# Kernel tuning notes

Hardware: AMD Instinct MI355X
Metric: run time of the kernel (lower is better)

The kernel has to match this reference:

```python
import jax, jax.numpy as jnp
import numpy as np

N_NODES = 1_000_000
N_EDGES = 16_000_000
F_IN, F_H1, F_H2, N_CLS = 32, 16, 8, 5
N_GRAPHS = 10_000


def setup_inputs() -> dict:
    key = jax.random.key(0)
    ks = jax.random.split(key, 10)
    x = jax.random.normal(ks[0], (N_NODES, F_IN), dtype=jnp.float32)
    edge_index = jax.random.randint(ks[1], (2, N_EDGES), 0, N_NODES, dtype=jnp.int32)
    batch = jnp.sort(jax.random.randint(ks[2], (N_NODES,), 0, N_GRAPHS, dtype=jnp.int32))
    # learned params (Glorot-ish scale)
    W1 = jax.random.normal(ks[3], (F_IN, F_H1), dtype=jnp.float32) / np.sqrt(F_IN)
    b1 = jnp.zeros((F_H1,), dtype=jnp.float32)
    W2 = jax.random.normal(ks[4], (F_H1, F_H2), dtype=jnp.float32) / np.sqrt(F_H1)
    b2 = jnp.zeros((F_H2,), dtype=jnp.float32)
    Wl = jax.random.normal(ks[5], (F_H2, N_CLS), dtype=jnp.float32) / np.sqrt(F_H2)
    bl = jnp.zeros((N_CLS,), dtype=jnp.float32)
    return {"x": x, "edge_index": edge_index, "batch": batch, "num_graphs": N_GRAPHS,
            "W1": W1, "b1": b1, "W2": W2, "b2": b2, "Wl": Wl, "bl": bl}


def _gcn_conv(x, W, b, src, dst, deg_inv_sqrt, norm_e, num_nodes):
    # h = X W, then symmetric-normalized aggregation with self loops:
    # out_i = sum_{(j->i)} norm_ji * h_j + deg_i^{-1} * h_i + b
    h = x @ W                                  # [N, F_out]
    msg = h[src] * norm_e[:, None]             # [E, F_out] gather + scale
    agg = jax.ops.segment_sum(msg, dst, num_segments=num_nodes)
    self_loop = h * (deg_inv_sqrt * deg_inv_sqrt)[:, None]
    return agg + self_loop + b


def reference(x, edge_index, batch, num_graphs, W1, b1, W2, b2, Wl, bl):
    num_nodes = x.shape[0]
    src, dst = edge_index[0], edge_index[1]
    # degrees including self loops (GCN: A_hat = A + I)
    deg = jax.ops.segment_sum(jnp.ones_like(dst, dtype=x.dtype), dst,
                              num_segments=num_nodes) + 1.0
    deg_inv_sqrt = jax.lax.rsqrt(deg)
    norm_e = deg_inv_sqrt[src] * deg_inv_sqrt[dst]   # [E]

    h = _gcn_conv(x, W1, b1, src, dst, deg_inv_sqrt, norm_e, num_nodes)
    h = jax.nn.relu(h)
    h = _gcn_conv(h, W2, b2, src, dst, deg_inv_sqrt, norm_e, num_nodes)
    h = jax.nn.relu(h)

    # global_mean_pool over graph ids
    sums = jax.ops.segment_sum(h, batch, num_segments=num_graphs)     # [G, F_H2]
    cnts = jax.ops.segment_sum(jnp.ones((num_nodes,), dtype=h.dtype), batch,
                               num_segments=num_graphs)
    pooled = sums / jnp.maximum(cnts, 1.0)[:, None]
    return pooled @ Wl + bl
```

## Files before the change

kernel.cpp:

```cpp
#include <hip/hip_runtime.h>


namespace {

constexpr int F_IN = 32, F_H1 = 16, F_H2 = 8, N_CLS = 5;
constexpr int BB = 10, NPB = 1 << BB;
constexpr int MAXB = 1024;
constexpr int CHUNK = 12288;


__global__ void k_mm1(const float* __restrict__ x, const float* __restrict__ W,
                      float* __restrict__ h, int N) {
  __shared__ float w[F_IN * F_H1];
  for (int k = threadIdx.x; k < F_IN * F_H1; k += blockDim.x) w[k] = W[k];
  __syncthreads();
  int i = blockIdx.x * blockDim.x + threadIdx.x;
  if (i >= N) return;
  const float4* xr = reinterpret_cast<const float4*>(x + (size_t)i * F_IN);
  float acc[F_H1];
#pragma unroll
  for (int f = 0; f < F_H1; ++f) acc[f] = 0.f;
#pragma unroll
  for (int k4 = 0; k4 < F_IN / 4; ++k4) {
    float4 v = xr[k4];
    float vv[4] = {v.x, v.y, v.z, v.w};
#pragma unroll
    for (int j = 0; j < 4; ++j) {
      const float* wr = &w[(k4 * 4 + j) * F_H1];
#pragma unroll
      for (int f = 0; f < F_H1; ++f) acc[f] = fmaf(vv[j], wr[f], acc[f]);
    }
  }
  float4* hr = reinterpret_cast<float4*>(h + (size_t)i * F_H1);
#pragma unroll
  for (int q = 0; q < F_H1 / 4; ++q)
    hr[q] = make_float4(acc[q * 4], acc[q * 4 + 1], acc[q * 4 + 2], acc[q * 4 + 3]);
}

__global__ void k_mm2(const float* __restrict__ in, const float* __restrict__ W,
                      float* __restrict__ h, int N) {
  __shared__ float w[F_H1 * F_H2];
  for (int k = threadIdx.x; k < F_H1 * F_H2; k += blockDim.x) w[k] = W[k];
  __syncthreads();
  int i = blockIdx.x * blockDim.x + threadIdx.x;
  if (i >= N) return;
  const float4* xr = reinterpret_cast<const float4*>(in + (size_t)i * F_H1);
  float acc[F_H2];
#pragma unroll
  for (int f = 0; f < F_H2; ++f) acc[f] = 0.f;
#pragma unroll
  for (int k4 = 0; k4 < F_H1 / 4; ++k4) {
    float4 v = xr[k4];
    float vv[4] = {v.x, v.y, v.z, v.w};
#pragma unroll
    for (int j = 0; j < 4; ++j) {
      const float* wr = &w[(k4 * 4 + j) * F_H2];
#pragma unroll
      for (int f = 0; f < F_H2; ++f) acc[f] = fmaf(vv[j], wr[f], acc[f]);
    }
  }
  float4* hr = reinterpret_cast<float4*>(h + (size_t)i * F_H2);
#pragma unroll
  for (int q = 0; q < F_H2 / 4; ++q)
    hr[q] = make_float4(acc[q * 4], acc[q * 4 + 1], acc[q * 4 + 2], acc[q * 4 + 3]);
}

__global__ void k_final(const float* __restrict__ pooled, const float* __restrict__ cnts,
                        const float* __restrict__ Wl, const float* __restrict__ bl,
                        float* __restrict__ out, int total) {
  int gid = blockIdx.x * blockDim.x + threadIdx.x;
  if (gid >= total) return;
  int g = gid / N_CLS, c = gid % N_CLS;
  float s = 0.f;
#pragma unroll
  for (int f = 0; f < F_H2; ++f) s += pooled[g * F_H2 + f] * Wl[f * N_CLS + c];
  out[gid] = s / fmaxf(cnts[g], 1.f) + bl[c];
}


__global__ void k_hist(const int* __restrict__ dst, int* __restrict__ bcnt,
                       int E, int nbuck) {
  __shared__ int h[MAXB];
  for (int i = threadIdx.x; i < MAXB; i += blockDim.x) h[i] = 0;
  __syncthreads();
  for (int e = blockIdx.x * blockDim.x + threadIdx.x; e < E;
       e += gridDim.x * blockDim.x)
    atomicAdd(&h[dst[e] >> BB], 1);
  __syncthreads();
  for (int i = threadIdx.x; i < nbuck; i += blockDim.x)
    if (h[i]) atomicAdd(&bcnt[i], h[i]);
}

__global__ void k_bscan(const int* __restrict__ bcnt, int* __restrict__ bbase,
                        int* __restrict__ bcur, int nbuck, int E) {
  __shared__ int s[MAXB];
  int t = threadIdx.x;
  int v = (t < nbuck) ? bcnt[t] : 0;
  s[t] = v;
  __syncthreads();
  for (int off = 1; off < MAXB; off <<= 1) {
    int x = (t >= off) ? s[t - off] : 0;
    __syncthreads();
    s[t] += x;
    __syncthreads();
  }
  int ex = s[t] - v;
  if (t < nbuck) { bbase[t] = ex; bcur[t] = ex; }
  if (t == 0) bbase[nbuck] = E;
}

__global__ __launch_bounds__(256)
void k_binscatter(const int* __restrict__ dst, const int* __restrict__ src,
                  int* __restrict__ bcur, int* __restrict__ packed, int E) {
  __shared__ int hist[MAXB];
  __shared__ int sbase[MAXB];
  __shared__ int lcur[MAXB];
  __shared__ int stg[CHUNK];
  __shared__ int stmp[256];
  int t = threadIdx.x;
  int c0 = blockIdx.x * CHUNK;
  int n = min(CHUNK, E - c0);
  for (int i = t; i < MAXB; i += 256) hist[i] = 0;
  __syncthreads();
  for (int j = t; j < n; j += 256) atomicAdd(&hist[dst[c0 + j] >> BB], 1);
  __syncthreads();
  int v[4], sum = 0;
  int b4 = t * 4;
#pragma unroll
  for (int k = 0; k < 4; ++k) { v[k] = hist[b4 + k]; sum += v[k]; }
  stmp[t] = sum;
  __syncthreads();
  for (int off = 1; off < 256; off <<= 1) {
    int x = (t >= off) ? stmp[t - off] : 0;
    __syncthreads();
    stmp[t] += x;
    __syncthreads();
  }
  int run = stmp[t] - sum;
#pragma unroll
  for (int k = 0; k < 4; ++k) { sbase[b4 + k] = run; lcur[b4 + k] = run; run += v[k]; }
  __syncthreads();
  for (int i = t; i < MAXB; i += 256) {
    int c = hist[i];
    if (c) hist[i] = atomicAdd(&bcur[i], c);
  }
  __syncthreads();
  for (int j = t; j < n; j += 256) {
    int d = dst[c0 + j], s = src[c0 + j];
    int b = d >> BB;
    int p = atomicAdd(&lcur[b], 1);
    stg[p] = ((d & (NPB - 1)) << 20) | s;
  }
  __syncthreads();
  for (int j = t; j < n; j += 256) {
    int lo = 0, hi = MAXB - 1;
    while (lo < hi) {
      int mid = (lo + hi + 1) >> 1;
      if (sbase[mid] <= j) lo = mid; else hi = mid - 1;
    }
    packed[hist[lo] + (j - sbase[lo])] = stg[j];
  }
}

__global__ void k_dis_b(const int* __restrict__ bbase, const int* __restrict__ packed,
                        float* __restrict__ dis, int N) {
  __shared__ int cnt[NPB];
  int t = threadIdx.x;
  for (int i = t; i < NPB; i += blockDim.x) cnt[i] = 0;
  __syncthreads();
  int b = blockIdx.x;
  int beg = bbase[b], end = bbase[b + 1];
  for (int e = beg + t; e < end; e += blockDim.x)
    atomicAdd(&cnt[packed[e] >> 20], 1);
  __syncthreads();
  int node0 = b << BB;
  for (int i = t; i < NPB; i += blockDim.x) {
    int node = node0 + i;
    if (node < N) dis[node] = rsqrtf((float)cnt[i] + 1.0f);
  }
}


template <int F>
__global__ __launch_bounds__(512)
void k_conv(const int* __restrict__ bbase, const int* __restrict__ packed,
            const float* __restrict__ dis, const float* __restrict__ h,
            const float* __restrict__ bias, float* __restrict__ out, int N) {
  __shared__ float acc[NPB * F];
  int t = threadIdx.x;
  for (int i = t; i < NPB * F; i += 512) acc[i] = 0.f;
  __syncthreads();
  int b = blockIdx.x;
  int beg = bbase[b], end = bbase[b + 1];
  const int EPI = 512 / F;
  int f = t % F, eg = t / F;
  for (int e = beg + eg; e < end; e += 2 * EPI) {
    int p0 = packed[e];
    int s0 = p0 & ((1 << 20) - 1), d0 = p0 >> 20;
    float m0 = dis[s0] * h[(size_t)s0 * F + f];
    int e1 = e + EPI;
    if (e1 < end) {
      int p1 = packed[e1];
      int s1 = p1 & ((1 << 20) - 1), d1 = p1 >> 20;
      float m1 = dis[s1] * h[(size_t)s1 * F + f];
      atomicAdd(&acc[d0 * F + f], m0);
      atomicAdd(&acc[d1 * F + f], m1);
    } else {
      atomicAdd(&acc[d0 * F + f], m0);
    }
  }
  __syncthreads();
  int node0 = b << BB;
  for (int i = t; i < NPB * F; i += 512) {
    int node = node0 + i / F;
    if (node >= N) continue;
    int ff = i % F;
    float di = dis[node];
    float v = fmaf(di, acc[i], fmaf(di * di, h[(size_t)node * F + ff], bias[ff]));
    out[(size_t)node * F + ff] = fmaxf(v, 0.f);
  }
}

__global__ __launch_bounds__(512)
void k_conv_pool(const int* __restrict__ bbase, const int* __restrict__ packed,
                 const float* __restrict__ dis, const float* __restrict__ h,
                 const float* __restrict__ bias, const int* __restrict__ batch,
                 float* __restrict__ pooled, float* __restrict__ cnts, int N) {
  constexpr int F = F_H2;
  __shared__ float acc[NPB * F];
  int t = threadIdx.x;
  for (int i = t; i < NPB * F; i += 512) acc[i] = 0.f;
  __syncthreads();
  int b = blockIdx.x;
  int beg = bbase[b], end = bbase[b + 1];
  const int EPI = 512 / F;
  int f = t % F, eg = t / F;
  for (int e = beg + eg; e < end; e += 2 * EPI) {
    int p0 = packed[e];
    int s0 = p0 & ((1 << 20) - 1), d0 = p0 >> 20;
    float m0 = dis[s0] * h[(size_t)s0 * F + f];
    int e1 = e + EPI;
    if (e1 < end) {
      int p1 = packed[e1];
      int s1 = p1 & ((1 << 20) - 1), d1 = p1 >> 20;
      float m1 = dis[s1] * h[(size_t)s1 * F + f];
      atomicAdd(&acc[d0 * F + f], m0);
      atomicAdd(&acc[d1 * F + f], m1);
    } else {
      atomicAdd(&acc[d0 * F + f], m0);
    }
  }
  __syncthreads();
  int node0 = b << BB;
  for (int i = t; i < NPB * F; i += 512) {
    int node = node0 + i / F;
    if (node >= N) continue;
    int ff = i % F;
    float di = dis[node];
    float v = fmaf(di, acc[i], fmaf(di * di, h[(size_t)node * F + ff], bias[ff]));
    v = fmaxf(v, 0.f);
    int g = batch[node];
    atomicAdd(&pooled[g * F_H2 + ff], v);
    if (ff == 0) atomicAdd(&cnts[g], 1.0f);
  }
}


__global__ void k_deg(const int* __restrict__ dst, float* __restrict__ deg, int E) {
  int e = blockIdx.x * blockDim.x + threadIdx.x;
  if (e < E) atomicAdd(&deg[dst[e]], 1.0f);
}
__global__ void k_dis(float* __restrict__ d, int N) {
  int i = blockIdx.x * blockDim.x + threadIdx.x;
  if (i < N) d[i] = rsqrtf(d[i] + 1.0f);
}
template <int F>
__global__ void k_edge(const int* __restrict__ src, const int* __restrict__ dst,
                       const float* __restrict__ dis, const float* __restrict__ h,
                       float* __restrict__ agg, int total) {
  int gid = blockIdx.x * blockDim.x + threadIdx.x;
  if (gid >= total) return;
  int e = gid / F, f = gid % F;
  int s = src[e], d = dst[e];
  atomicAdd(&agg[d * F + f], h[s * F + f] * dis[s] * dis[d]);
}
template <int F>
__global__ void k_combine(const float* __restrict__ h, const float* __restrict__ dis,
                          const float* __restrict__ b, float* __restrict__ agg, int total) {
  int gid = blockIdx.x * blockDim.x + threadIdx.x;
  if (gid >= total) return;
  int i = gid / F, f = gid % F;
  float di = dis[i];
  agg[gid] = fmaxf(agg[gid] + h[gid] * di * di + b[f], 0.f);
}
__global__ void k_combine_pool_fb(const float* __restrict__ h2, const float* __restrict__ agg2,
                                  const float* __restrict__ dis, const float* __restrict__ b,
                                  const int* __restrict__ batch, float* __restrict__ pooled,
                                  float* __restrict__ cnts, int total) {
  int gid = blockIdx.x * blockDim.x + threadIdx.x;
  if (gid >= total) return;
  int i = gid >> 3, f = gid & 7;
  float di = dis[i];
  float v = fmaxf(agg2[gid] + h2[gid] * di * di + b[f], 0.f);
  int g = batch[i];
  atomicAdd(&pooled[g * F_H2 + f], v);
  if (f == 0) atomicAdd(&cnts[g], 1.0f);
}

}

extern "C" void kernel_launch(void* const* d_in, const int* in_sizes, int n_in,
                              void* d_out, int out_size, void* d_ws, size_t ws_size,
                              hipStream_t stream) {
  const float* x   = (const float*)d_in[0];
  const int* ei    = (const int*)d_in[1];
  const int* batch = (const int*)d_in[2];
  const float* W1 = (const float*)d_in[4];
  const float* b1 = (const float*)d_in[5];
  const float* W2 = (const float*)d_in[6];
  const float* b2 = (const float*)d_in[7];
  const float* Wl = (const float*)d_in[8];
  const float* bl = (const float*)d_in[9];

  const int N = in_sizes[0] / F_IN;
  const int E = in_sizes[1] / 2;
  const int G = out_size / N_CLS;
  const int* src  = ei;
  const int* dstp = ei + E;

  const int BLK = 256;
  const int nbuck = (N + NPB - 1) >> BB;

  size_t need = (size_t)(3 * MAXB + 8) * 4
              + (size_t)E * 4
              + (size_t)N * 4
              + (size_t)N * F_H1 * 4
              + (size_t)N * F_H1 * 4
              + (size_t)G * (F_H2 + 1) * 4 + 1024;

  if (N <= (1 << 20) && nbuck <= MAXB && ws_size >= need) {
    char* p = (char*)d_ws;
    int*   bcnt   = (int*)p;    p += (size_t)MAXB * 4;
    int*   bbase  = (int*)p;    p += (size_t)(MAXB + 4) * 4;
    int*   bcur   = (int*)p;    p += (size_t)MAXB * 4;
    int*   packed = (int*)p;    p += (size_t)E * 4;
    float* dis    = (float*)p;  p += (size_t)N * 4;
    float* H      = (float*)p;  p += (size_t)N * F_H1 * 4;
    float* O      = (float*)p;  p += (size_t)N * F_H1 * 4;
    float* pooled = (float*)p;  p += (size_t)G * F_H2 * 4;
    float* cnts   = (float*)p;

    hipMemsetAsync(bcnt, 0, (size_t)MAXB * 4, stream);
    hipMemsetAsync(pooled, 0, ((size_t)G * F_H2 + G) * 4, stream);

    k_hist<<<2048, BLK, 0, stream>>>(dstp, bcnt, E, nbuck);
    k_bscan<<<1, MAXB, 0, stream>>>(bcnt, bbase, bcur, nbuck, E);
    k_binscatter<<<(E + CHUNK - 1) / CHUNK, BLK, 0, stream>>>(dstp, src, bcur, packed, E);
    k_dis_b<<<nbuck, BLK, 0, stream>>>(bbase, packed, dis, N);

    k_mm1<<<(N + BLK - 1) / BLK, BLK, 0, stream>>>(x, W1, H, N);
    k_conv<F_H1><<<nbuck, 512, 0, stream>>>(bbase, packed, dis, H, b1, O, N);
    k_mm2<<<(N + BLK - 1) / BLK, BLK, 0, stream>>>(O, W2, H, N);
    k_conv_pool<<<nbuck, 512, 0, stream>>>(bbase, packed, dis, H, b2, batch,
                                           pooled, cnts, N);

    k_final<<<(G * N_CLS + BLK - 1) / BLK, BLK, 0, stream>>>(
        pooled, cnts, Wl, bl, (float*)d_out, G * N_CLS);
    return;
  }

  float* ws = (float*)d_ws;
  float* dis    = ws;
  float* A      = ws + N;
  float* B      = A + (size_t)N * F_H1;
  float* h2     = A;
  float* agg2   = A + (size_t)N * F_H2;
  float* pooled = B + (size_t)N * F_H1;
  float* cnts   = pooled + (size_t)G * F_H2;

  hipMemsetAsync(dis, 0, (size_t)N * sizeof(float), stream);
  hipMemsetAsync(B, 0, (size_t)N * F_H1 * sizeof(float), stream);
  hipMemsetAsync(pooled, 0, ((size_t)G * F_H2 + G) * sizeof(float), stream);

  k_deg<<<(E + BLK - 1) / BLK, BLK, 0, stream>>>(dstp, dis, E);
  k_dis<<<(N + BLK - 1) / BLK, BLK, 0, stream>>>(dis, N);
  k_mm1<<<(N + BLK - 1) / BLK, BLK, 0, stream>>>(x, W1, A, N);
  k_edge<F_H1><<<(E * F_H1 + BLK - 1) / BLK, BLK, 0, stream>>>(src, dstp, dis, A, B, E * F_H1);
  k_combine<F_H1><<<(N * F_H1 + BLK - 1) / BLK, BLK, 0, stream>>>(A, dis, b1, B, N * F_H1);
  hipMemsetAsync(agg2, 0, (size_t)N * F_H2 * sizeof(float), stream);
  k_mm2<<<(N + BLK - 1) / BLK, BLK, 0, stream>>>(B, W2, h2, N);
  k_edge<F_H2><<<(E * F_H2 + BLK - 1) / BLK, BLK, 0, stream>>>(src, dstp, dis, h2, agg2, E * F_H2);
  k_combine_pool_fb<<<(N * F_H2 + BLK - 1) / BLK, BLK, 0, stream>>>(
      h2, agg2, dis, b2, batch, pooled, cnts, N * F_H2);
  k_final<<<(G * N_CLS + BLK - 1) / BLK, BLK, 0, stream>>>(
      pooled, cnts, Wl, bl, (float*)d_out, G * N_CLS);
}
```

Baseline: 2.882 ms.

## Prescale features by inverse-sqrt degree, shrink buckets, unroll gathers, add nontemporal loads

The matmul kernels now multiply each node's output row by its inverse-sqrt degree, so the edge loop gathers only the prescaled feature and no longer reads dis per source. The shared accumulator starts from the node's own prescaled row, which makes the self-loop term fall out of the algebra. Bucket width drops to 512 nodes with 2048 buckets and smaller scatter chunks, the scan is adapted to cover them, and the edge loop is unrolled four-deep to keep more gathers in flight. Nontemporal loads and stores and an occupancy launch bound are added, which may change cache behaviour and register pressure.

```diff
diff --git a/kernel.cpp b/kernel.cpp
--- a/kernel.cpp
+++ b/kernel.cpp
@@ -4,25 +4,27 @@
 namespace {
 
 constexpr int F_IN = 32, F_H1 = 16, F_H2 = 8, N_CLS = 5;
-constexpr int BB = 10, NPB = 1 << BB;
-constexpr int MAXB = 1024;
-constexpr int CHUNK = 12288;
+constexpr int BB = 9, NPB = 1 << BB;
+constexpr int MAXB = 2048;
+constexpr int CHUNK = 8192;
+
+typedef float v4f __attribute__((ext_vector_type(4)));
 
 
 __global__ void k_mm1(const float* __restrict__ x, const float* __restrict__ W,
-                      float* __restrict__ h, int N) {
+                      const float* __restrict__ dis, float* __restrict__ hp, int N) {
   __shared__ float w[F_IN * F_H1];
   for (int k = threadIdx.x; k < F_IN * F_H1; k += blockDim.x) w[k] = W[k];
   __syncthreads();
   int i = blockIdx.x * blockDim.x + threadIdx.x;
   if (i >= N) return;
-  const float4* xr = reinterpret_cast<const float4*>(x + (size_t)i * F_IN);
+  const v4f* xr = reinterpret_cast<const v4f*>(x + (size_t)i * F_IN);
   float acc[F_H1];
 #pragma unroll
   for (int f = 0; f < F_H1; ++f) acc[f] = 0.f;
 #pragma unroll
   for (int k4 = 0; k4 < F_IN / 4; ++k4) {
-    float4 v = xr[k4];
+    v4f v = __builtin_nontemporal_load(&xr[k4]);
     float vv[4] = {v.x, v.y, v.z, v.w};
 #pragma unroll
     for (int j = 0; j < 4; ++j) {
@@ -31,26 +33,33 @@
       for (int f = 0; f < F_H1; ++f) acc[f] = fmaf(vv[j], wr[f], acc[f]);
     }
   }
-  float4* hr = reinterpret_cast<float4*>(h + (size_t)i * F_H1);
-#pragma unroll
-  for (int q = 0; q < F_H1 / 4; ++q)
-    hr[q] = make_float4(acc[q * 4], acc[q * 4 + 1], acc[q * 4 + 2], acc[q * 4 + 3]);
+  float di = dis ? dis[i] : 1.f;
+  v4f* hr = reinterpret_cast<v4f*>(hp + (size_t)i * F_H1);
+#pragma unroll
+  for (int q = 0; q < F_H1 / 4; ++q) {
+    v4f r;
+    r.x = di * acc[q * 4];
+    r.y = di * acc[q * 4 + 1];
+    r.z = di * acc[q * 4 + 2];
+    r.w = di * acc[q * 4 + 3];
+    hr[q] = r;
+  }
 }
 
 __global__ void k_mm2(const float* __restrict__ in, const float* __restrict__ W,
-                      float* __restrict__ h, int N) {
+                      const float* __restrict__ dis, float* __restrict__ hp, int N) {
   __shared__ float w[F_H1 * F_H2];
   for (int k = threadIdx.x; k < F_H1 * F_H2; k += blockDim.x) w[k] = W[k];
   __syncthreads();
   int i = blockIdx.x * blockDim.x + threadIdx.x;
   if (i >= N) return;
-  const float4* xr = reinterpret_cast<const float4*>(in + (size_t)i * F_H1);
+  const v4f* xr = reinterpret_cast<const v4f*>(in + (size_t)i * F_H1);
   float acc[F_H2];
 #pragma unroll
   for (int f = 0; f < F_H2; ++f) acc[f] = 0.f;
 #pragma unroll
   for (int k4 = 0; k4 < F_H1 / 4; ++k4) {
-    float4 v = xr[k4];
+    v4f v = __builtin_nontemporal_load(&xr[k4]);
     float vv[4] = {v.x, v.y, v.z, v.w};
 #pragma unroll
     for (int j = 0; j < 4; ++j) {
@@ -59,10 +68,17 @@
       for (int f = 0; f < F_H2; ++f) acc[f] = fmaf(vv[j], wr[f], acc[f]);
     }
   }
-  float4* hr = reinterpret_cast<float4*>(h + (size_t)i * F_H2);
-#pragma unroll
-  for (int q = 0; q < F_H2 / 4; ++q)
-    hr[q] = make_float4(acc[q * 4], acc[q * 4 + 1], acc[q * 4 + 2], acc[q * 4 + 3]);
+  float di = dis ? dis[i] : 1.f;
+  v4f* hr = reinterpret_cast<v4f*>(hp + (size_t)i * F_H2);
+#pragma unroll
+  for (int q = 0; q < F_H2 / 4; ++q) {
+    v4f r;
+    r.x = di * acc[q * 4];
+    r.y = di * acc[q * 4 + 1];
+    r.z = di * acc[q * 4 + 2];
+    r.w = di * acc[q * 4 + 3];
+    hr[q] = r;
+  }
 }
 
 __global__ void k_final(const float* __restrict__ pooled, const float* __restrict__ cnts,
@@ -85,7 +101,7 @@
   __syncthreads();
   for (int e = blockIdx.x * blockDim.x + threadIdx.x; e < E;
        e += gridDim.x * blockDim.x)
-    atomicAdd(&h[dst[e] >> BB], 1);
+    atomicAdd(&h[__builtin_nontemporal_load(&dst[e]) >> BB], 1);
   __syncthreads();
   for (int i = threadIdx.x; i < nbuck; i += blockDim.x)
     if (h[i]) atomicAdd(&bcnt[i], h[i]);
@@ -93,19 +109,23 @@
 
 __global__ void k_bscan(const int* __restrict__ bcnt, int* __restrict__ bbase,
                         int* __restrict__ bcur, int nbuck, int E) {
-  __shared__ int s[MAXB];
+  __shared__ int stmp[1024];
   int t = threadIdx.x;
-  int v = (t < nbuck) ? bcnt[t] : 0;
-  s[t] = v;
-  __syncthreads();
-  for (int off = 1; off < MAXB; off <<= 1) {
-    int x = (t >= off) ? s[t - off] : 0;
+  int i0 = t * 2;
+  int v0 = (i0 < nbuck) ? bcnt[i0] : 0;
+  int v1 = (i0 + 1 < nbuck) ? bcnt[i0 + 1] : 0;
+  int sum = v0 + v1;
+  stmp[t] = sum;
+  __syncthreads();
+  for (int off = 1; off < 1024; off <<= 1) {
+    int x = (t >= off) ? stmp[t - off] : 0;
     __syncthreads();
-    s[t] += x;
+    stmp[t] += x;
     __syncthreads();
   }
-  int ex = s[t] - v;
-  if (t < nbuck) { bbase[t] = ex; bcur[t] = ex; }
+  int run = stmp[t] - sum;
+  if (i0 < nbuck) { bbase[i0] = run; bcur[i0] = run; }
+  if (i0 + 1 < nbuck) { bbase[i0 + 1] = run + v0; bcur[i0 + 1] = run + v0; }
   if (t == 0) bbase[nbuck] = E;
 }
 
@@ -122,12 +142,13 @@
   int n = min(CHUNK, E - c0);
   for (int i = t; i < MAXB; i += 256) hist[i] = 0;
   __syncthreads();
-  for (int j = t; j < n; j += 256) atomicAdd(&hist[dst[c0 + j] >> BB], 1);
-  __syncthreads();
-  int v[4], sum = 0;
-  int b4 = t * 4;
-#pragma unroll
-  for (int k = 0; k < 4; ++k) { v[k] = hist[b4 + k]; sum += v[k]; }
+  for (int j = t; j < n; j += 256)
+    atomicAdd(&hist[__builtin_nontemporal_load(&dst[c0 + j]) >> BB], 1);
+  __syncthreads();
+  int v[8], sum = 0;
+  int b8 = t * 8;
+#pragma unroll
+  for (int k = 0; k < 8; ++k) { v[k] = hist[b8 + k]; sum += v[k]; }
   stmp[t] = sum;
   __syncthreads();
   for (int off = 1; off < 256; off <<= 1) {
@@ -138,7 +159,7 @@
   }
   int run = stmp[t] - sum;
 #pragma unroll
-  for (int k = 0; k < 4; ++k) { sbase[b4 + k] = run; lcur[b4 + k] = run; run += v[k]; }
+  for (int k = 0; k < 8; ++k) { sbase[b8 + k] = run; lcur[b8 + k] = run; run += v[k]; }
   __syncthreads();
   for (int i = t; i < MAXB; i += 256) {
     int c = hist[i];
@@ -146,7 +167,8 @@
   }
   __syncthreads();
   for (int j = t; j < n; j += 256) {
-    int d = dst[c0 + j], s = src[c0 + j];
+    int d = __builtin_nontemporal_load(&dst[c0 + j]);
+    int s = __builtin_nontemporal_load(&src[c0 + j]);
     int b = d >> BB;
     int p = atomicAdd(&lcur[b], 1);
     stg[p] = ((d & (NPB - 1)) << 20) | s;
@@ -171,7 +193,7 @@
   int b = blockIdx.x;
   int beg = bbase[b], end = bbase[b + 1];
   for (int e = beg + t; e < end; e += blockDim.x)
-    atomicAdd(&cnt[packed[e] >> 20], 1);
+    atomicAdd(&cnt[__builtin_nontemporal_load(&packed[e]) >> 20], 1);
   __syncthreads();
   int node0 = b << BB;
   for (int i = t; i < NPB; i += blockDim.x) {
@@ -182,83 +204,106 @@
 
 
 template <int F>
-__global__ __launch_bounds__(512)
+__global__ __launch_bounds__(512, 8)
 void k_conv(const int* __restrict__ bbase, const int* __restrict__ packed,
-            const float* __restrict__ dis, const float* __restrict__ h,
+            const float* __restrict__ dis, const float* __restrict__ hp,
             const float* __restrict__ bias, float* __restrict__ out, int N) {
   __shared__ float acc[NPB * F];
   int t = threadIdx.x;
-  for (int i = t; i < NPB * F; i += 512) acc[i] = 0.f;
-  __syncthreads();
   int b = blockIdx.x;
+  int node0 = b << BB;
+  for (int i4 = t; i4 < NPB * F / 4; i4 += 512) {
+    int idx = i4 * 4;
+    int node = node0 + idx / F;
+    v4f v = {0.f, 0.f, 0.f, 0.f};
+    if (node < N) v = *reinterpret_cast<const v4f*>(hp + (size_t)node0 * F + idx);
+    *reinterpret_cast<v4f*>(&acc[idx]) = v;
+  }
+  __syncthreads();
   int beg = bbase[b], end = bbase[b + 1];
   const int EPI = 512 / F;
   int f = t % F, eg = t / F;
-  for (int e = beg + eg; e < end; e += 2 * EPI) {
-    int p0 = packed[e];
-    int s0 = p0 & ((1 << 20) - 1), d0 = p0 >> 20;
-    float m0 = dis[s0] * h[(size_t)s0 * F + f];
-    int e1 = e + EPI;
-    if (e1 < end) {
-      int p1 = packed[e1];
-      int s1 = p1 & ((1 << 20) - 1), d1 = p1 >> 20;
-      float m1 = dis[s1] * h[(size_t)s1 * F + f];
-      atomicAdd(&acc[d0 * F + f], m0);
-      atomicAdd(&acc[d1 * F + f], m1);
-    } else {
-      atomicAdd(&acc[d0 * F + f], m0);
-    }
-  }
-  __syncthreads();
+  for (int e = beg + eg; e < end; e += 4 * EPI) {
+    int pe[4]; float hv[4]; int dl[4]; bool ok[4];
+#pragma unroll
+    for (int u = 0; u < 4; ++u) {
+      int ee = e + u * EPI;
+      ok[u] = ee < end;
+      pe[u] = ok[u] ? __builtin_nontemporal_load(&packed[ee]) : 0;
+    }
+#pragma unroll
+    for (int u = 0; u < 4; ++u) {
+      int s = pe[u] & 0xFFFFF;
+      dl[u] = pe[u] >> 20;
+      hv[u] = ok[u] ? hp[(size_t)s * F + f] : 0.f;
+    }
+#pragma unroll
+    for (int u = 0; u < 4; ++u)
+      if (ok[u]) atomicAdd(&acc[dl[u] * F + f], hv[u]);
+  }
+  __syncthreads();
+  for (int i4 = t; i4 < NPB * F / 4; i4 += 512) {
+    int idx = i4 * 4;
+    int node = node0 + idx / F;
+    if (node >= N) continue;
+    int ff = idx % F;
+    float di = dis[node];
+    v4f a = *reinterpret_cast<const v4f*>(&acc[idx]);
+    v4f r;
+    r.x = fmaxf(fmaf(di, a.x, bias[ff + 0]), 0.f);
+    r.y = fmaxf(fmaf(di, a.y, bias[ff + 1]), 0.f);
+    r.z = fmaxf(fmaf(di, a.z, bias[ff + 2]), 0.f);
+    r.w = fmaxf(fmaf(di, a.w, bias[ff + 3]), 0.f);
+    __builtin_nontemporal_store(r, reinterpret_cast<v4f*>(out + (size_t)node0 * F + idx));
+  }
+}
+
+__global__ __launch_bounds__(512, 8)
+void k_conv_pool(const int* __restrict__ bbase, const int* __restrict__ packed,
+                 const float* __restrict__ dis, const float* __restrict__ hp,
+                 const float* __restrict__ bias, const int* __restrict__ batch,
+                 float* __restrict__ pooled, float* __restrict__ cnts, int N) {
+  constexpr int F = F_H2;
+  __shared__ float acc[NPB * F];
+  int t = threadIdx.x;
+  int b = blockIdx.x;
   int node0 = b << BB;
+  for (int i4 = t; i4 < NPB * F / 4; i4 += 512) {
+    int idx = i4 * 4;
+    int node = node0 + idx / F;
+    v4f v = {0.f, 0.f, 0.f, 0.f};
+    if (node < N) v = *reinterpret_cast<const v4f*>(hp + (size_t)node0 * F + idx);
+    *reinterpret_cast<v4f*>(&acc[idx]) = v;
+  }
+  __syncthreads();
+  int beg = bbase[b], end = bbase[b + 1];
+  const int EPI = 512 / F;
+  int f = t % F, eg = t / F;
+  for (int e = beg + eg; e < end; e += 4 * EPI) {
+    int pe[4]; float hv[4]; int dl[4]; bool ok[4];
+#pragma unroll
+    for (int u = 0; u < 4; ++u) {
+      int ee = e + u * EPI;
+      ok[u] = ee < end;
+      pe[u] = ok[u] ? __builtin_nontemporal_load(&packed[ee]) : 0;
+    }
+#pragma unroll
+    for (int u = 0; u < 4; ++u) {
+      int s = pe[u] & 0xFFFFF;
+      dl[u] = pe[u] >> 20;
+      hv[u] = ok[u] ? hp[(size_t)s * F + f] : 0.f;
+    }
+#pragma unroll
+    for (int u = 0; u < 4; ++u)
+      if (ok[u]) atomicAdd(&acc[dl[u] * F + f], hv[u]);
+  }
+  __syncthreads();
   for (int i = t; i < NPB * F; i += 512) {
     int node = node0 + i / F;
     if (node >= N) continue;
     int ff = i % F;
     float di = dis[node];
-    float v = fmaf(di, acc[i], fmaf(di * di, h[(size_t)node * F + ff], bias[ff]));
-    out[(size_t)node * F + ff] = fmaxf(v, 0.f);
-  }
-}
-
-__global__ __launch_bounds__(512)
-void k_conv_pool(const int* __restrict__ bbase, const int* __restrict__ packed,
-                 const float* __restrict__ dis, const float* __restrict__ h,
-                 const float* __restrict__ bias, const int* __restrict__ batch,
-                 float* __restrict__ pooled, float* __restrict__ cnts, int N) {
-  constexpr int F = F_H2;
-  __shared__ float acc[NPB * F];
-  int t = threadIdx.x;
-  for (int i = t; i < NPB * F; i += 512) acc[i] = 0.f;
-  __syncthreads();
-  int b = blockIdx.x;
-  int beg = bbase[b], end = bbase[b + 1];
-  const int EPI = 512 / F;
-  int f = t % F, eg = t / F;
-  for (int e = beg + eg; e < end; e += 2 * EPI) {
-    int p0 = packed[e];
-    int s0 = p0 & ((1 << 20) - 1), d0 = p0 >> 20;
-    float m0 = dis[s0] * h[(size_t)s0 * F + f];
-    int e1 = e + EPI;
-    if (e1 < end) {
-      int p1 = packed[e1];
-      int s1 = p1 & ((1 << 20) - 1), d1 = p1 >> 20;
-      float m1 = dis[s1] * h[(size_t)s1 * F + f];
-      atomicAdd(&acc[d0 * F + f], m0);
-      atomicAdd(&acc[d1 * F + f], m1);
-    } else {
-      atomicAdd(&acc[d0 * F + f], m0);
-    }
-  }
-  __syncthreads();
-  int node0 = b << BB;
-  for (int i = t; i < NPB * F; i += 512) {
-    int node = node0 + i / F;
-    if (node >= N) continue;
-    int ff = i % F;
-    float di = dis[node];
-    float v = fmaf(di, acc[i], fmaf(di * di, h[(size_t)node * F + ff], bias[ff]));
-    v = fmaxf(v, 0.f);
+    float v = fmaxf(fmaf(di, acc[i], bias[ff]), 0.f);
     int g = batch[node];
     atomicAdd(&pooled[g * F_H2 + ff], v);
     if (ff == 0) atomicAdd(&cnts[g], 1.0f);
@@ -350,17 +395,17 @@
     float* pooled = (float*)p;  p += (size_t)G * F_H2 * 4;
     float* cnts   = (float*)p;
 
-    hipMemsetAsync(bcnt, 0, (size_t)MAXB * 4, stream);
-    hipMemsetAsync(pooled, 0, ((size_t)G * F_H2 + G) * 4, stream);
+    (void)hipMemsetAsync(bcnt, 0, (size_t)MAXB * 4, stream);
+    (void)hipMemsetAsync(pooled, 0, ((size_t)G * F_H2 + G) * 4, stream);
 
     k_hist<<<2048, BLK, 0, stream>>>(dstp, bcnt, E, nbuck);
-    k_bscan<<<1, MAXB, 0, stream>>>(bcnt, bbase, bcur, nbuck, E);
+    k_bscan<<<1, 1024, 0, stream>>>(bcnt, bbase, bcur, nbuck, E);
     k_binscatter<<<(E + CHUNK - 1) / CHUNK, BLK, 0, stream>>>(dstp, src, bcur, packed, E);
     k_dis_b<<<nbuck, BLK, 0, stream>>>(bbase, packed, dis, N);
 
-    k_mm1<<<(N + BLK - 1) / BLK, BLK, 0, stream>>>(x, W1, H, N);
+    k_mm1<<<(N + BLK - 1) / BLK, BLK, 0, stream>>>(x, W1, dis, H, N);
     k_conv<F_H1><<<nbuck, 512, 0, stream>>>(bbase, packed, dis, H, b1, O, N);
-    k_mm2<<<(N + BLK - 1) / BLK, BLK, 0, stream>>>(O, W2, H, N);
+    k_mm2<<<(N + BLK - 1) / BLK, BLK, 0, stream>>>(O, W2, dis, H, N);
     k_conv_pool<<<nbuck, 512, 0, stream>>>(bbase, packed, dis, H, b2, batch,
                                            pooled, cnts, N);
 
@@ -378,17 +423,17 @@
   float* pooled = B + (size_t)N * F_H1;
   float* cnts   = pooled + (size_t)G * F_H2;
 
-  hipMemsetAsync(dis, 0, (size_t)N * sizeof(float), stream);
-  hipMemsetAsync(B, 0, (size_t)N * F_H1 * sizeof(float), stream);
-  hipMemsetAsync(pooled, 0, ((size_t)G * F_H2 + G) * sizeof(float), stream);
+  (void)hipMemsetAsync(dis, 0, (size_t)N * sizeof(float), stream);
+  (void)hipMemsetAsync(B, 0, (size_t)N * F_H1 * sizeof(float), stream);
+  (void)hipMemsetAsync(pooled, 0, ((size_t)G * F_H2 + G) * sizeof(float), stream);
 
   k_deg<<<(E + BLK - 1) / BLK, BLK, 0, stream>>>(dstp, dis, E);
   k_dis<<<(N + BLK - 1) / BLK, BLK, 0, stream>>>(dis, N);
-  k_mm1<<<(N + BLK - 1) / BLK, BLK, 0, stream>>>(x, W1, A, N);
+  k_mm1<<<(N + BLK - 1) / BLK, BLK, 0, stream>>>(x, W1, nullptr, A, N);
   k_edge<F_H1><<<(E * F_H1 + BLK - 1) / BLK, BLK, 0, stream>>>(src, dstp, dis, A, B, E * F_H1);
   k_combine<F_H1><<<(N * F_H1 + BLK - 1) / BLK, BLK, 0, stream>>>(A, dis, b1, B, N * F_H1);
-  hipMemsetAsync(agg2, 0, (size_t)N * F_H2 * sizeof(float), stream);
-  k_mm2<<<(N + BLK - 1) / BLK, BLK, 0, stream>>>(B, W2, h2, N);
+  (void)hipMemsetAsync(agg2, 0, (size_t)N * F_H2 * sizeof(float), stream);
+  k_mm2<<<(N + BLK - 1) / BLK, BLK, 0, stream>>>(B, W2, nullptr, h2, N);
   k_edge<F_H2><<<(E * F_H2 + BLK - 1) / BLK, BLK, 0, stream>>>(src, dstp, dis, h2, agg2, E * F_H2);
   k_combine_pool_fb<<<(N * F_H2 + BLK - 1) / BLK, BLK, 0, stream>>>(
       h2, agg2, dis, b2, batch, pooled, cnts, N * F_H2);
```

Result: slower. 3.520 ms (+22.1%).
